# Kernel optimization log

Hardware: AMD Instinct MI355X
Metric: run time of the kernel (lower is better)

The kernel has to match this reference:

```python
import jax, jax.numpy as jnp
import numpy as np

N, H, W, K = 4, 512, 512, 8
V, F = 50000, 100000
SIGMA, GAMMA = 1e-4, 1e-4
ZNEAR, ZFAR = 1.0, 100.0
EPS = 1e-10


def setup_inputs() -> dict:
    key = jax.random.key(0)
    k1, k2, k3, k4, k5, k6 = jax.random.split(key, 6)
    vn = jax.random.normal(k1, (V, 3), dtype=jnp.float32)
    verts_normals = vn / jnp.linalg.norm(vn, axis=-1, keepdims=True)
    bary = jax.random.uniform(k2, (N, H, W, K, 3), dtype=jnp.float32)
    bary_coords = bary / bary.sum(-1, keepdims=True)  # valid barycentrics
    dists = jax.random.normal(k3, (N, H, W, K), dtype=jnp.float32) * 1e-4
    zbuf = jax.random.uniform(k4, (N, H, W, K), dtype=jnp.float32) * (ZFAR - ZNEAR) + ZNEAR
    faces = jax.random.randint(k5, (F, 3), 0, V, dtype=jnp.int64)
    # include -1 entries (background pixels), as in real rasterizer output
    pix_to_face = jax.random.randint(k6, (N, H, W, K), -1, F, dtype=jnp.int64)
    return {"verts_normals": verts_normals, "bary_coords": bary_coords,
            "dists": dists, "zbuf": zbuf, "faces": faces,
            "pix_to_face": pix_to_face}


def reference(verts_normals, bary_coords, dists, zbuf, faces, pix_to_face):
    # --- normal_shading: gather + barycentric interpolation of vertex normals ---
    faces_normals = verts_normals[faces]                      # (F, 3verts, 3)
    mask = pix_to_face >= 0                                   # (N,H,W,K)
    idx = jnp.where(mask, pix_to_face, 0)
    attrs = faces_normals[idx]                                # (N,H,W,K,3verts,3)
    colors = jnp.einsum('nhwkv,nhwkvc->nhwkc', bary_coords, attrs)
    colors = colors * mask[..., None]                         # zero masked pixels
    opacity = jnp.ones(mask.shape, dtype=colors.dtype)        # torch.ones_like
    # --- softmax_rgb_blend ---
    maskf = mask.astype(colors.dtype)
    prob_map = jax.nn.sigmoid(-dists / SIGMA) * maskf
    alpha = jnp.prod(1.0 - prob_map, axis=-1)                 # (N,H,W)
    z_inv = (ZFAR - zbuf) / (ZFAR - ZNEAR) * maskf
    z_inv_max = jnp.max(z_inv, axis=-1, keepdims=True)
    weights_num = prob_map * jnp.exp((z_inv - z_inv_max) / GAMMA) * opacity
    delta = jnp.maximum(jnp.exp((EPS - z_inv_max) / GAMMA), EPS)
    denom = weights_num.sum(-1, keepdims=True) + delta        # (N,H,W,1)
    background = jnp.array([1.0, 1.0, 1.0], dtype=colors.dtype)
    weighted_colors = jnp.einsum('nhwk,nhwkc->nhwc', weights_num, colors)
    rgb = (weighted_colors + delta * background) / denom      # (N,H,W,3)
    a = (1.0 - alpha)[..., None]                              # (N,H,W,1)
    return jnp.concatenate([rgb, a], axis=-1)                 # (N,H,W,4)
```

## Files before the change

kernel.cpp:

```cpp
#include <hip/hip_runtime.h>


constexpr int   N_PIX      = 4 * 512 * 512;
constexpr float INV_SIGMA  = 1.0f / 1e-4f;
constexpr float INV_GAMMA  = 1.0f / 1e-4f;
constexpr float ZFARV      = 100.0f;
constexpr float INV_ZRANGE = 1.0f / 99.0f;
constexpr float EPSV       = 1e-10f;

__global__ __launch_bounds__(256)
void build_face_normals_kernel(const float* __restrict__ vn,
                               const int*   __restrict__ faces,
                               float*       __restrict__ fn,
                               int nf)
{
    int f = blockIdx.x * blockDim.x + threadIdx.x;
    if (f >= nf) return;
    int v0 = faces[3 * f + 0];
    int v1 = faces[3 * f + 1];
    int v2 = faces[3 * f + 2];
    const float* p0 = vn + 3 * (size_t)v0;
    const float* p1 = vn + 3 * (size_t)v1;
    const float* p2 = vn + 3 * (size_t)v2;
    float4 r0 = make_float4(p0[0], p0[1], p0[2], p1[0]);
    float4 r1 = make_float4(p1[1], p1[2], p2[0], p2[1]);
    float4 r2 = make_float4(p2[2], 0.f, 0.f, 0.f);
    float4* dst = reinterpret_cast<float4*>(fn + 12 * (size_t)f);
    dst[0] = r0; dst[1] = r1; dst[2] = r2;
}

__global__ __launch_bounds__(256)
void shade_kernel(const float* __restrict__ bary,
                  const float* __restrict__ dists,
                  const float* __restrict__ zbuf,
                  const int*   __restrict__ p2f,
                  const float* __restrict__ fn,
                  const float* __restrict__ vn,
                  const int*   __restrict__ faces,
                  float*       __restrict__ out)
{
    int pix = blockIdx.x * blockDim.x + threadIdx.x;
    if (pix >= N_PIX) return;

    const float4* dptr = reinterpret_cast<const float4*>(dists + 8 * (size_t)pix);
    const float4* zptr = reinterpret_cast<const float4*>(zbuf  + 8 * (size_t)pix);
    const int4*   fptr = reinterpret_cast<const int4*>(p2f     + 8 * (size_t)pix);
    const float4* bptr = reinterpret_cast<const float4*>(bary  + 24 * (size_t)pix);

    float4 d0 = dptr[0], d1 = dptr[1];
    float4 z0 = zptr[0], z1 = zptr[1];
    int4   f0 = fptr[0], f1 = fptr[1];
    float4 b0 = bptr[0], b1 = bptr[1], b2 = bptr[2];
    float4 b3 = bptr[3], b4 = bptr[4], b5 = bptr[5];

    float dk[8] = {d0.x, d0.y, d0.z, d0.w, d1.x, d1.y, d1.z, d1.w};
    float zk[8] = {z0.x, z0.y, z0.z, z0.w, z1.x, z1.y, z1.z, z1.w};
    int   fk[8] = {f0.x, f0.y, f0.z, f0.w, f1.x, f1.y, f1.z, f1.w};
    float bf[24] = {b0.x, b0.y, b0.z, b0.w, b1.x, b1.y, b1.z, b1.w,
                    b2.x, b2.y, b2.z, b2.w, b3.x, b3.y, b3.z, b3.w,
                    b4.x, b4.y, b4.z, b4.w, b5.x, b5.y, b5.z, b5.w};

    float prob[8], zinv[8];
    float zmax  = 0.0f;
    float alpha = 1.0f;
#pragma unroll
    for (int k = 0; k < 8; ++k) {
        bool  m  = fk[k] >= 0;
        float pr = m ? __builtin_amdgcn_rcpf(1.0f + __expf(dk[k] * INV_SIGMA)) : 0.0f;
        prob[k]  = pr;
        alpha   *= (1.0f - pr);
        float zi = m ? (ZFARV - zk[k]) * INV_ZRANGE : 0.0f;
        zinv[k]  = zi;
        zmax     = fmaxf(zmax, zi);
    }

    float wsum = 0.0f, cr = 0.0f, cg = 0.0f, cb = 0.0f;
#pragma unroll
    for (int k = 0; k < 8; ++k) {
        float w = prob[k] * __expf((zinv[k] - zmax) * INV_GAMMA);
        if (w != 0.0f) {
            int idx = fk[k] < 0 ? 0 : fk[k];
            float n0x, n0y, n0z, n1x, n1y, n1z, n2x, n2y, n2z;
            if (fn) {
                const float4* fr = reinterpret_cast<const float4*>(fn + 12 * (size_t)idx);
                float4 r0 = fr[0], r1 = fr[1], r2 = fr[2];
                n0x = r0.x; n0y = r0.y; n0z = r0.z;
                n1x = r0.w; n1y = r1.x; n1z = r1.y;
                n2x = r1.z; n2y = r1.w; n2z = r2.x;
            } else {
                int v0 = faces[3 * idx + 0];
                int v1 = faces[3 * idx + 1];
                int v2 = faces[3 * idx + 2];
                n0x = vn[3 * v0 + 0]; n0y = vn[3 * v0 + 1]; n0z = vn[3 * v0 + 2];
                n1x = vn[3 * v1 + 0]; n1y = vn[3 * v1 + 1]; n1z = vn[3 * v1 + 2];
                n2x = vn[3 * v2 + 0]; n2y = vn[3 * v2 + 1]; n2z = vn[3 * v2 + 2];
            }
            float bw0 = bf[3 * k + 0], bw1 = bf[3 * k + 1], bw2 = bf[3 * k + 2];
            cr += w * (bw0 * n0x + bw1 * n1x + bw2 * n2x);
            cg += w * (bw0 * n0y + bw1 * n1y + bw2 * n2y);
            cb += w * (bw0 * n0z + bw1 * n1z + bw2 * n2z);
        }
        wsum += w;
    }

    float delta     = fmaxf(__expf((EPSV - zmax) * INV_GAMMA), EPSV);
    float inv_denom = 1.0f / (wsum + delta);

    float4 o;
    o.x = (cr + delta) * inv_denom;
    o.y = (cg + delta) * inv_denom;
    o.z = (cb + delta) * inv_denom;
    o.w = 1.0f - alpha;
    reinterpret_cast<float4*>(out)[pix] = o;
}

extern "C" void kernel_launch(void* const* d_in, const int* in_sizes, int n_in,
                              void* d_out, int out_size, void* d_ws, size_t ws_size,
                              hipStream_t stream) {
    const float* vn    = (const float*)d_in[0];
    const float* bary  = (const float*)d_in[1];
    const float* dists = (const float*)d_in[2];
    const float* zbuf  = (const float*)d_in[3];
    const int*   faces = (const int*)d_in[4];
    const int*   p2f   = (const int*)d_in[5];
    float*       out   = (float*)d_out;

    int nf = in_sizes[4] / 3;

    float* fn = nullptr;
    size_t need = (size_t)nf * 12 * sizeof(float);
    if (ws_size >= need) {
        fn = (float*)d_ws;
        build_face_normals_kernel<<<(nf + 255) / 256, 256, 0, stream>>>(vn, faces, fn, nf);
    }

    shade_kernel<<<N_PIX / 256, 256, 0, stream>>>(bary, dists, zbuf, p2f,
                                                  fn, vn, faces, out);
}
```

Measured before the change: 235.6 us.

## Assign one thread per fragment with lane-shuffle reductions across K

Moves the shading kernel from one thread per pixel to one thread per fragment, with eight lanes per pixel. The max, product and sum over K become xor-shuffle reductions, and lane 0 writes the output. This gives eight times more threads and coalesced scalar loads, so more of the scattered face-normal gathers can be in flight at once. The cost is the shuffle instructions, some duplicated per-pixel work, and an output store made by only one lane in eight.

```diff
diff --git a/kernel.cpp b/kernel.cpp
--- a/kernel.cpp
+++ b/kernel.cpp
@@ -2,6 +2,7 @@
 
 
 constexpr int   N_PIX      = 4 * 512 * 512;
+constexpr int   N_FRAG     = N_PIX * 8;
 constexpr float INV_SIGMA  = 1.0f / 1e-4f;
 constexpr float INV_GAMMA  = 1.0f / 1e-4f;
 constexpr float ZFARV      = 100.0f;
@@ -39,79 +40,74 @@
                   const int*   __restrict__ faces,
                   float*       __restrict__ out)
 {
-    int pix = blockIdx.x * blockDim.x + threadIdx.x;
-    if (pix >= N_PIX) return;
+    int gid = blockIdx.x * blockDim.x + threadIdx.x;
+    if (gid >= N_FRAG) return;
+    int kk  = gid & 7;
+    int pix = gid >> 3;
 
-    const float4* dptr = reinterpret_cast<const float4*>(dists + 8 * (size_t)pix);
-    const float4* zptr = reinterpret_cast<const float4*>(zbuf  + 8 * (size_t)pix);
-    const int4*   fptr = reinterpret_cast<const int4*>(p2f     + 8 * (size_t)pix);
-    const float4* bptr = reinterpret_cast<const float4*>(bary  + 24 * (size_t)pix);
+    float d  = dists[gid];
+    float zb = zbuf[gid];
+    int   f  = p2f[gid];
 
-    float4 d0 = dptr[0], d1 = dptr[1];
-    float4 z0 = zptr[0], z1 = zptr[1];
-    int4   f0 = fptr[0], f1 = fptr[1];
-    float4 b0 = bptr[0], b1 = bptr[1], b2 = bptr[2];
-    float4 b3 = bptr[3], b4 = bptr[4], b5 = bptr[5];
+    bool  m  = f >= 0;
+    float pr = m ? __builtin_amdgcn_rcpf(1.0f + __expf(d * INV_SIGMA)) : 0.0f;
+    float zi = m ? (ZFARV - zb) * INV_ZRANGE : 0.0f;
 
-    float dk[8] = {d0.x, d0.y, d0.z, d0.w, d1.x, d1.y, d1.z, d1.w};
-    float zk[8] = {z0.x, z0.y, z0.z, z0.w, z1.x, z1.y, z1.z, z1.w};
-    int   fk[8] = {f0.x, f0.y, f0.z, f0.w, f1.x, f1.y, f1.z, f1.w};
-    float bf[24] = {b0.x, b0.y, b0.z, b0.w, b1.x, b1.y, b1.z, b1.w,
-                    b2.x, b2.y, b2.z, b2.w, b3.x, b3.y, b3.z, b3.w,
-                    b4.x, b4.y, b4.z, b4.w, b5.x, b5.y, b5.z, b5.w};
+    float zmax = zi;
+    zmax = fmaxf(zmax, __shfl_xor(zmax, 1));
+    zmax = fmaxf(zmax, __shfl_xor(zmax, 2));
+    zmax = fmaxf(zmax, __shfl_xor(zmax, 4));
 
-    float prob[8], zinv[8];
-    float zmax  = 0.0f;
-    float alpha = 1.0f;
-#pragma unroll
-    for (int k = 0; k < 8; ++k) {
-        bool  m  = fk[k] >= 0;
-        float pr = m ? __builtin_amdgcn_rcpf(1.0f + __expf(dk[k] * INV_SIGMA)) : 0.0f;
-        prob[k]  = pr;
-        alpha   *= (1.0f - pr);
-        float zi = m ? (ZFARV - zk[k]) * INV_ZRANGE : 0.0f;
-        zinv[k]  = zi;
-        zmax     = fmaxf(zmax, zi);
+    float am = 1.0f - pr;
+    am *= __shfl_xor(am, 1);
+    am *= __shfl_xor(am, 2);
+    am *= __shfl_xor(am, 4);
+
+    float w = pr * __expf((zi - zmax) * INV_GAMMA);
+
+    float cr = 0.0f, cg = 0.0f, cb = 0.0f;
+    if (w != 0.0f) {
+        float b0 = bary[3 * (size_t)gid + 0];
+        float b1 = bary[3 * (size_t)gid + 1];
+        float b2 = bary[3 * (size_t)gid + 2];
+        float n0x, n0y, n0z, n1x, n1y, n1z, n2x, n2y, n2z;
+        if (fn) {
+            const float4* fr = reinterpret_cast<const float4*>(fn + 12 * (size_t)f);
+            float4 r0 = fr[0], r1 = fr[1], r2 = fr[2];
+            n0x = r0.x; n0y = r0.y; n0z = r0.z;
+            n1x = r0.w; n1y = r1.x; n1z = r1.y;
+            n2x = r1.z; n2y = r1.w; n2z = r2.x;
+        } else {
+            int v0 = faces[3 * f + 0];
+            int v1 = faces[3 * f + 1];
+            int v2 = faces[3 * f + 2];
+            n0x = vn[3 * v0 + 0]; n0y = vn[3 * v0 + 1]; n0z = vn[3 * v0 + 2];
+            n1x = vn[3 * v1 + 0]; n1y = vn[3 * v1 + 1]; n1z = vn[3 * v1 + 2];
+            n2x = vn[3 * v2 + 0]; n2y = vn[3 * v2 + 1]; n2z = vn[3 * v2 + 2];
+        }
+        cr = w * (b0 * n0x + b1 * n1x + b2 * n2x);
+        cg = w * (b0 * n0y + b1 * n1y + b2 * n2y);
+        cb = w * (b0 * n0z + b1 * n1z + b2 * n2z);
     }
 
-    float wsum = 0.0f, cr = 0.0f, cg = 0.0f, cb = 0.0f;
-#pragma unroll
-    for (int k = 0; k < 8; ++k) {
-        float w = prob[k] * __expf((zinv[k] - zmax) * INV_GAMMA);
-        if (w != 0.0f) {
-            int idx = fk[k] < 0 ? 0 : fk[k];
-            float n0x, n0y, n0z, n1x, n1y, n1z, n2x, n2y, n2z;
-            if (fn) {
-                const float4* fr = reinterpret_cast<const float4*>(fn + 12 * (size_t)idx);
-                float4 r0 = fr[0], r1 = fr[1], r2 = fr[2];
-                n0x = r0.x; n0y = r0.y; n0z = r0.z;
-                n1x = r0.w; n1y = r1.x; n1z = r1.y;
-                n2x = r1.z; n2y = r1.w; n2z = r2.x;
-            } else {
-                int v0 = faces[3 * idx + 0];
-                int v1 = faces[3 * idx + 1];
-                int v2 = faces[3 * idx + 2];
-                n0x = vn[3 * v0 + 0]; n0y = vn[3 * v0 + 1]; n0z = vn[3 * v0 + 2];
-                n1x = vn[3 * v1 + 0]; n1y = vn[3 * v1 + 1]; n1z = vn[3 * v1 + 2];
-                n2x = vn[3 * v2 + 0]; n2y = vn[3 * v2 + 1]; n2z = vn[3 * v2 + 2];
-            }
-            float bw0 = bf[3 * k + 0], bw1 = bf[3 * k + 1], bw2 = bf[3 * k + 2];
-            cr += w * (bw0 * n0x + bw1 * n1x + bw2 * n2x);
-            cg += w * (bw0 * n0y + bw1 * n1y + bw2 * n2y);
-            cb += w * (bw0 * n0z + bw1 * n1z + bw2 * n2z);
-        }
-        wsum += w;
+    float ws = w;
+    ws += __shfl_xor(ws, 1);  cr += __shfl_xor(cr, 1);
+    cg += __shfl_xor(cg, 1);  cb += __shfl_xor(cb, 1);
+    ws += __shfl_xor(ws, 2);  cr += __shfl_xor(cr, 2);
+    cg += __shfl_xor(cg, 2);  cb += __shfl_xor(cb, 2);
+    ws += __shfl_xor(ws, 4);  cr += __shfl_xor(cr, 4);
+    cg += __shfl_xor(cg, 4);  cb += __shfl_xor(cb, 4);
+
+    if (kk == 0) {
+        float delta     = fmaxf(__expf((EPSV - zmax) * INV_GAMMA), EPSV);
+        float inv_denom = __builtin_amdgcn_rcpf(ws + delta);
+        float4 o;
+        o.x = (cr + delta) * inv_denom;
+        o.y = (cg + delta) * inv_denom;
+        o.z = (cb + delta) * inv_denom;
+        o.w = 1.0f - am;
+        reinterpret_cast<float4*>(out)[pix] = o;
     }
-
-    float delta     = fmaxf(__expf((EPSV - zmax) * INV_GAMMA), EPSV);
-    float inv_denom = 1.0f / (wsum + delta);
-
-    float4 o;
-    o.x = (cr + delta) * inv_denom;
-    o.y = (cg + delta) * inv_denom;
-    o.z = (cb + delta) * inv_denom;
-    o.w = 1.0f - alpha;
-    reinterpret_cast<float4*>(out)[pix] = o;
 }
 
 extern "C" void kernel_launch(void* const* d_in, const int* in_sizes, int n_in,
@@ -134,6 +130,6 @@
         build_face_normals_kernel<<<(nf + 255) / 256, 256, 0, stream>>>(vn, faces, fn, nf);
     }
 
-    shade_kernel<<<N_PIX / 256, 256, 0, stream>>>(bary, dists, zbuf, p2f,
-                                                  fn, vn, faces, out);
+    shade_kernel<<<N_FRAG / 256, 256, 0, stream>>>(bary, dists, zbuf, p2f,
+                                                   fn, vn, faces, out);
 }
```

After: 228.2 us. -3.1%, faster.
